# Performance work log

Measured on AMD Instinct MI355X. Metric: run time of the kernel, lower is better.

Reference implementation:

```python
import jax, jax.numpy as jnp
import numpy as np

N, D, E, H = 1024, 256, 16, 8
HD = D // H
F = 4 * D  # GatedMLP intermediate
SCALE = 1.0 / np.sqrt(HD)
EPS = 1e-6


def rmsnorm(x, w):
    rms = jnp.sqrt(jnp.mean(x * x, axis=-1, keepdims=True) + EPS)
    return x / rms * w


def mha(x, wq, wk, wv, wo, mask=None, edge_bias=None):
    # x: [N, D]; weights stored (in, out) so y = x @ W
    q = (x @ wq).reshape(N, H, HD).transpose(1, 0, 2)  # [H, N, HD]
    k = (x @ wk).reshape(N, H, HD).transpose(1, 0, 2)
    v = (x @ wv).reshape(N, H, HD).transpose(1, 0, 2)
    scores = jnp.einsum('hnd,hmd->hnm', q, k) * SCALE  # [H, N, N]
    if edge_bias is not None:
        scores = scores + edge_bias.transpose(2, 0, 1)
    if mask is not None:
        scores = jnp.where(mask[None, :, :], scores, -jnp.inf)
    attn = jax.nn.softmax(scores, axis=-1)
    attn = jnp.nan_to_num(attn, nan=0.0)
    out = jnp.einsum('hnm,hmd->hnd', attn, v)  # [H, N, HD]
    out = out.transpose(1, 0, 2).reshape(N, D)
    return out @ wo


def setup_inputs() -> dict:
    key = jax.random.key(0)
    ks = jax.random.split(key, 40)
    i = iter(range(40))

    def g(shape, s=0.02):
        return (jax.random.normal(ks[next(i)], shape) * s).astype(jnp.float32)

    inp = {
        'features': jax.random.normal(ks[next(i)], (N, D), dtype=jnp.float32),
        'adjacency': jax.random.randint(ks[next(i)], (N, N), 0, 2, dtype=jnp.int32),
        'edge_features': jax.random.normal(ks[next(i)], (N, N, E), dtype=jnp.float32),
        'role_indices': jax.random.randint(ks[next(i)], (N,), 0, 16, dtype=jnp.int64),
        'role_norm_w': jnp.ones((D,), jnp.float32),
        'role_q_w': g((D, D)), 'role_k_w': g((D, D)), 'role_v_w': g((D, D)), 'role_o_w': g((D, D)),
        'nb_norm_w': jnp.ones((D,), jnp.float32),
        'nb_q_w': g((D, D)), 'nb_k_w': g((D, D)), 'nb_v_w': g((D, D)), 'nb_o_w': g((D, D)),
        'edge_w1': g((E, D)), 'edge_b1': jnp.zeros((D,), jnp.float32),
        'edge_w2': g((D, H)), 'edge_b2': jnp.zeros((H,), jnp.float32),
        'full_norm_w': jnp.ones((D,), jnp.float32),
        'full_q_w': g((D, D)), 'full_k_w': g((D, D)), 'full_v_w': g((D, D)), 'full_o_w': g((D, D)),
        'feat_norm_w': jnp.ones((D,), jnp.float32),
        'feat_t_w': g((D, D)), 'feat_t_b': jnp.zeros((D,), jnp.float32),
        'feat_g_w': g((2 * D, D)), 'feat_g_b': jnp.zeros((D,), jnp.float32),
        'ffn_norm_w': jnp.ones((D,), jnp.float32),
        'ffn_gate_w': g((D, F)), 'ffn_up_w': g((D, F)), 'ffn_down_w': g((F, D)),
    }
    return inp


def reference(features, adjacency, edge_features, role_indices,
              role_norm_w, role_q_w, role_k_w, role_v_w, role_o_w,
              nb_norm_w, nb_q_w, nb_k_w, nb_v_w, nb_o_w,
              edge_w1, edge_b1, edge_w2, edge_b2,
              full_norm_w, full_q_w, full_k_w, full_v_w, full_o_w,
              feat_norm_w, feat_t_w, feat_t_b, feat_g_w, feat_g_b,
              ffn_norm_w, ffn_gate_w, ffn_up_w, ffn_down_w):
    # masks (dropout is identity in eval mode)
    role_mask = role_indices[:, None] == role_indices[None, :]          # [N, N]
    neighbor_mask = (adjacency > 0) | jnp.eye(N, dtype=bool)            # [N, N]

    x = features
    # 1. role attention
    x = x + mha(rmsnorm(x, role_norm_w), role_q_w, role_k_w, role_v_w, role_o_w, mask=role_mask)
    # 2. neighbor attention with per-head edge bias from MLP over edge features
    hdn = jax.nn.silu(edge_features @ edge_w1 + edge_b1)                # [N, N, D]
    edge_bias = hdn @ edge_w2 + edge_b2                                 # [N, N, H]
    x = x + mha(rmsnorm(x, nb_norm_w), nb_q_w, nb_k_w, nb_v_w, nb_o_w, mask=neighbor_mask, edge_bias=edge_bias)
    # 3. full attention
    x = x + mha(rmsnorm(x, full_norm_w), full_q_w, full_k_w, full_v_w, full_o_w)
    # 4. feature mixing (gated residual)
    xn = rmsnorm(x, feat_norm_w)
    t = jax.nn.silu(xn @ feat_t_w + feat_t_b)
    gate = jax.nn.sigmoid(jnp.concatenate([xn, t], axis=-1) @ feat_g_w + feat_g_b)
    x = x + gate * t
    # 5. gated FFN
    xn = rmsnorm(x, ffn_norm_w)
    x = x + (jax.nn.silu(xn @ ffn_gate_w) * (xn @ ffn_up_w)) @ ffn_down_w
    return x
```

## Files before the change

### kernel.cpp

```cpp
#include <hip/hip_runtime.h>
#include <math.h>

#define N 1024
#define D 256
#define E 16
#define H 8
#define HD 32
#define F 1024
#define NN (1024 * 1024)
#define SCALE 0.17677669529663687f
#define EPS 1e-6f

typedef unsigned short u16;
typedef __attribute__((ext_vector_type(8))) short bfrag8;
typedef __attribute__((ext_vector_type(4))) float accf4;

__device__ __forceinline__ float block_sum(float v) {
    #pragma unroll
    for (int off = 32; off > 0; off >>= 1) v += __shfl_xor(v, off);
    __shared__ float ws[4];
    if ((threadIdx.x & 63) == 0) ws[threadIdx.x >> 6] = v;
    __syncthreads();
    v = ws[0] + ws[1] + ws[2] + ws[3];
    __syncthreads();
    return v;
}

__device__ __forceinline__ float silu_f(float x) { return x / (1.f + __expf(-x)); }
__device__ __forceinline__ float sigmoid_f(float x) { return 1.f / (1.f + __expf(-x)); }

__device__ __forceinline__ u16 f2bf(float x) {
    union { float f; unsigned int u; } c;
    c.f = x;
    unsigned int r = c.u + 0x7fffu + ((c.u >> 16) & 1u);
    return (u16)(r >> 16);
}

__device__ __forceinline__ unsigned int cvt_pk_bf16(float a, float b) {
    unsigned int r;
    asm("v_cvt_pk_bf16_f32 %0, %1, %2" : "=v"(r) : "v"(a), "v"(b));
    return r;
}

__global__ void copy4_kernel(const float4* __restrict__ a, float4* __restrict__ b, int n4) {
    int i = blockIdx.x * 256 + threadIdx.x;
    if (i < n4) b[i] = a[i];
}

__global__ void gate_combine_kernel(const float* __restrict__ g, const float* __restrict__ t,
                                    float* __restrict__ x, int n) {
    int i = blockIdx.x * 256 + threadIdx.x;
    if (i < n) x[i] += sigmoid_f(g[i]) * t[i];
}

__global__ void cvt_bf16_kernel(const float* __restrict__ in, u16* __restrict__ out, int n) {
    int i = blockIdx.x * 256 + threadIdx.x;
    if (i < n) out[i] = f2bf(in[i]);
}

__global__ void ffn_mulcvt_kernel(const float* __restrict__ guv, u16* __restrict__ hb) {
    int i = blockIdx.x * 256 + threadIdx.x;
    int j = i >> 10, f = i & 1023;
    float g = guv[(long)j * 2048 + f];
    float u = guv[(long)j * 2048 + 1024 + f];
    hb[i] = f2bf(silu_f(g) * u);
}

__global__ void rmsnorm_bf16_kernel(const float* __restrict__ x, const float* __restrict__ w,
                                    u16* __restrict__ out) {
    int row = blockIdx.x;
    int t = threadIdx.x;
    float v = x[(long)row * D + t];
    float s = block_sum(v * v);
    float rms = sqrtf(s * (1.f / D) + EPS);
    out[(long)row * D + t] = f2bf(v / rms * w[t]);
}

__global__ void transpose_bf16_kernel(const float* __restrict__ in, long ldin,
                                      u16* __restrict__ out, int K, int Nc) {
    __shared__ float tile[32][33];
    int k0 = blockIdx.y * 32, n0 = blockIdx.x * 32;
    int c = threadIdx.x & 31, r8 = threadIdx.x >> 5;
    #pragma unroll
    for (int i = 0; i < 4; i++) {
        int r = r8 + i * 8;
        tile[r][c] = in[(long)(k0 + r) * ldin + n0 + c];
    }
    __syncthreads();
    #pragma unroll
    for (int i = 0; i < 4; i++) {
        int r = r8 + i * 8;
        out[(long)(n0 + r) * K + k0 + c] = f2bf(tile[c][r]);
    }
}

template <int NTW, int ACT, bool ACCUM, bool BIAS, bool BF16O>
__global__ __launch_bounds__(256) void bgemm_kernel(
    const u16* __restrict__ A, const u16* __restrict__ B, const float* __restrict__ bias,
    void* __restrict__ C, int M, int K, int Nc, int ldc, long sA, long sB, long sC) {
    constexpr int NTILE = NTW * 16;
    __shared__ __align__(16) u16 Asm[64 * 72];
    __shared__ __align__(16) u16 Bsm[NTILE * 72];
    A += (long)blockIdx.z * sA;
    B += (long)blockIdx.z * sB;
    long cbase = (long)blockIdx.z * sC;
    int m0 = blockIdx.y * 64, n0 = blockIdx.x * NTILE;
    int t = threadIdx.x;
    int wave = t >> 6, lane = t & 63, lg = lane >> 4, lr = lane & 15;
    accf4 acc[NTW] = {};
    for (int k0 = 0; k0 < K; k0 += 64) {
        #pragma unroll
        for (int c = 0; c < 2; c++) {
            int flat = c * 4096 + t * 16;
            int row = flat >> 7, col = (flat & 127) >> 1;
            *(int4*)&Asm[row * 72 + col] = *(const int4*)&A[(long)(m0 + row) * K + k0 + col];
        }
        #pragma unroll
        for (int c = 0; c < NTW / 2; c++) {
            int flat = c * 4096 + t * 16;
            int row = flat >> 7, col = (flat & 127) >> 1;
            *(int4*)&Bsm[row * 72 + col] = *(const int4*)&B[(long)(n0 + row) * K + k0 + col];
        }
        __syncthreads();
        #pragma unroll
        for (int ks = 0; ks < 2; ks++) {
            bfrag8 af = *(const bfrag8*)&Asm[(wave * 16 + lr) * 72 + ks * 32 + lg * 8];
            #pragma unroll
            for (int nt = 0; nt < NTW; nt++) {
                bfrag8 bf = *(const bfrag8*)&Bsm[(nt * 16 + lr) * 72 + ks * 32 + lg * 8];
                acc[nt] = __builtin_amdgcn_mfma_f32_16x16x32_bf16(af, bf, acc[nt], 0, 0, 0);
            }
        }
        __syncthreads();
    }
    float* Cf = (float*)C;
    u16* Cb = (u16*)C;
    #pragma unroll
    for (int nt = 0; nt < NTW; nt++) {
        int gn = n0 + nt * 16 + lr;
        #pragma unroll
        for (int r = 0; r < 4; r++) {
            int gm = m0 + wave * 16 + lg * 4 + r;
            float v = acc[nt][r];
            if (BIAS) v += bias[gn];
            if (ACT == 1) v = silu_f(v);
            long idx = cbase + (long)gm * ldc + gn;
            if (BF16O) Cb[idx] = f2bf(v);
            else if (ACCUM) Cf[idx] += v;
            else Cf[idx] = v;
        }
    }
}

template <int MASK>
__global__ __launch_bounds__(256) void flash_attn_kernel(
    const u16* __restrict__ qkvbf, const u16* __restrict__ vbt,
    const float* __restrict__ ebT, const int* __restrict__ roles,
    const int* __restrict__ adj, u16* __restrict__ aob) {
    __shared__ int roles_s[N];
    __shared__ __align__(16) u16 P_lds[4][16][72];
    __shared__ float mrg_m[4][16], mrg_l[4][16];
    __shared__ __align__(16) float mrg_O[2][32][16];

    int h = blockIdx.y;
    int t = threadIdx.x, wave = t >> 6, lane = t & 63;
    int lg = lane >> 4, lr = lane & 15;
    int iw = wave >> 1, jh = wave & 1;
    int i = blockIdx.x * 32 + iw * 16 + lr;

    if (MASK == 1) {
        #pragma unroll
        for (int c = 0; c < 4; c++) roles_s[t + c * 256] = roles[t + c * 256];
    }
    __syncthreads();

    bfrag8 qf = *(const bfrag8*)&qkvbf[(long)i * 768 + h * HD + lg * 8];
    int role_i = (MASK == 1) ? roles_s[i] : 0;

    accf4 o0 = {0.f, 0.f, 0.f, 0.f}, o1 = {0.f, 0.f, 0.f, 0.f};
    float m_run = -1e30f, l_run = 0.f;

    for (int jt = 0; jt < 8; jt++) {
        int j0 = jh * 512 + jt * 64;
        float p[16];
        float tmax = -1e30f;
        #pragma unroll
        for (int js = 0; js < 4; js++) {
            bfrag8 kf = *(const bfrag8*)&qkvbf[(long)(j0 + js * 16 + lr) * 768 + 256 + h * HD + lg * 8];
            accf4 z = {0.f, 0.f, 0.f, 0.f};
            accf4 s = __builtin_amdgcn_mfma_f32_16x16x32_bf16(kf, qf, z, 0, 0, 0);
            float4 eb4;
            int4 ad4;
            if (MASK == 2) {
                eb4 = *(const float4*)&ebT[(long)h * NN + (long)i * N + j0 + js * 16 + lg * 4];
                ad4 = *(const int4*)&adj[(long)i * N + j0 + js * 16 + lg * 4];
            }
            #pragma unroll
            for (int r = 0; r < 4; r++) {
                int j = j0 + js * 16 + lg * 4 + r;
                float val = s[r] * SCALE;
                bool keep = true;
                if (MASK == 2) {
                    val += (r == 0) ? eb4.x : (r == 1) ? eb4.y : (r == 2) ? eb4.z : eb4.w;
                    int av = (r == 0) ? ad4.x : (r == 1) ? ad4.y : (r == 2) ? ad4.z : ad4.w;
                    keep = (av > 0) || (i == j);
                }
                if (MASK == 1) keep = (roles_s[j] == role_i);
                val = keep ? val : -1e30f;
                p[js * 4 + r] = val;
                tmax = fmaxf(tmax, val);
            }
        }
        tmax = fmaxf(tmax, __shfl_xor(tmax, 16));
        tmax = fmaxf(tmax, __shfl_xor(tmax, 32));
        float m_new = fmaxf(m_run, tmax);
        float alpha = __expf(m_run - m_new);
        float lsum = 0.f;
        #pragma unroll
        for (int v = 0; v < 16; v++) {
            float pe = __expf(p[v] - m_new);
            p[v] = pe;
            lsum += pe;
        }
        lsum += __shfl_xor(lsum, 16);
        lsum += __shfl_xor(lsum, 32);
        l_run = l_run * alpha + lsum;
        m_run = m_new;
        #pragma unroll
        for (int r = 0; r < 4; r++) { o0[r] *= alpha; o1[r] *= alpha; }
        #pragma unroll
        for (int js = 0; js < 4; js++) {
            uint2 pk;
            pk.x = cvt_pk_bf16(p[js * 4 + 0], p[js * 4 + 1]);
            pk.y = cvt_pk_bf16(p[js * 4 + 2], p[js * 4 + 3]);
            *(uint2*)&P_lds[wave][lr][js * 16 + lg * 4] = pk;
        }
        #pragma unroll
        for (int ks = 0; ks < 2; ks++) {
            bfrag8 pb = *(const bfrag8*)&P_lds[wave][lr][ks * 32 + lg * 8];
            bfrag8 v0 = *(const bfrag8*)&vbt[(long)(h * HD + lr) * N + j0 + ks * 32 + lg * 8];
            bfrag8 v1 = *(const bfrag8*)&vbt[(long)(h * HD + 16 + lr) * N + j0 + ks * 32 + lg * 8];
            o0 = __builtin_amdgcn_mfma_f32_16x16x32_bf16(v0, pb, o0, 0, 0, 0);
            o1 = __builtin_amdgcn_mfma_f32_16x16x32_bf16(v1, pb, o1, 0, 0, 0);
        }
    }

    if (lg == 0) { mrg_m[wave][lr] = m_run; mrg_l[wave][lr] = l_run; }
    __syncthreads();
    int other = wave ^ 1;
    float m_o = mrg_m[other][lr], l_o = mrg_l[other][lr];
    float m_tot = fmaxf(m_run, m_o);
    float a_s = __expf(m_run - m_tot);
    float a_o = __expf(m_o - m_tot);
    float inv = 1.f / (a_s * l_run + a_o * l_o);
    if (jh == 0) {
        #pragma unroll
        for (int r = 0; r < 4; r++) {
            mrg_O[iw][lg * 4 + r][lr] = a_s * o0[r];
            mrg_O[iw][16 + lg * 4 + r][lr] = a_s * o1[r];
        }
    }
    __syncthreads();
    if (jh == 1) {
        #pragma unroll
        for (int r = 0; r < 4; r++) {
            float f0 = (mrg_O[iw][lg * 4 + r][lr] + a_s * o0[r]) * inv;
            float f1 = (mrg_O[iw][16 + lg * 4 + r][lr] + a_s * o1[r]) * inv;
            aob[(long)i * D + h * HD + lg * 4 + r] = f2bf(f0);
            aob[(long)i * D + h * HD + 16 + lg * 4 + r] = f2bf(f1);
        }
    }
}

__global__ __launch_bounds__(256, 3) void edge_mlp_mfma_kernel(
    const float* __restrict__ ef, const float* __restrict__ w1, const float* __restrict__ b1,
    const float* __restrict__ w2, const float* __restrict__ b2, float* __restrict__ ebT) {
    __shared__ __align__(16) u16 w1t[256 * 16];
    __shared__ __align__(16) u16 w2t[16 * 256];
    __shared__ __align__(16) u16 hid[4][16 * 264];
    int t = threadIdx.x;
    int i = blockIdx.x;

    {
        int d = t;
        #pragma unroll
        for (int e = 0; e < 16; e++) w1t[d * 16 + e] = f2bf(w1[e * 256 + d]);
        float4 wa = *(const float4*)&w2[d * 8];
        float4 wb = *(const float4*)&w2[d * 8 + 4];
        w2t[0 * 256 + d] = f2bf(wa.x);
        w2t[1 * 256 + d] = f2bf(wa.y);
        w2t[2 * 256 + d] = f2bf(wa.z);
        w2t[3 * 256 + d] = f2bf(wa.w);
        w2t[4 * 256 + d] = f2bf(wb.x);
        w2t[5 * 256 + d] = f2bf(wb.y);
        w2t[6 * 256 + d] = f2bf(wb.z);
        w2t[7 * 256 + d] = f2bf(wb.w);
        #pragma unroll
        for (int h = 8; h < 16; h++) w2t[h * 256 + d] = 0;
    }
    __syncthreads();

    int wave = t >> 6, lane = t & 63;
    int lg = lane >> 4, lr = lane & 15;
    u16* hw = hid[wave];

    bfrag8 a1[16];
    #pragma unroll
    for (int dt = 0; dt < 16; dt++) {
        int d = dt * 16 + lr;
        if (lg < 2) {
            a1[dt] = *(const bfrag8*)&w1t[d * 16 + lg * 8];
        } else if (lg == 2) {
            union { unsigned int u[4]; bfrag8 s; } z = {{0u, 0u, 0u, 0u}};
            z.u[0] = (unsigned int)f2bf(b1[d]);
            a1[dt] = z.s;
        } else {
            union { unsigned int u[4]; bfrag8 s; } z = {{0u, 0u, 0u, 0u}};
            a1[dt] = z.s;
        }
    }
    bfrag8 a2[8];
    #pragma unroll
    for (int ks = 0; ks < 8; ks++)
        a2[ks] = *(const bfrag8*)&w2t[lr * 256 + ks * 32 + lg * 8];

    float b2v[4];
    #pragma unroll
    for (int r = 0; r < 4; r++) b2v[r] = (lg < 2) ? b2[lg * 4 + r] : 0.f;

    for (int it = 0; it < 16; it++) {
        long rowbase = (long)i * N + (it * 4 + wave) * 16;
        bfrag8 bfrag;
        if (lg < 2) {
            const float* p = &ef[(rowbase + lr) * E + lg * 8];
            float4 f0 = *(const float4*)p;
            float4 f1 = *(const float4*)(p + 4);
            union { unsigned int u[4]; bfrag8 s; } uu;
            uu.u[0] = cvt_pk_bf16(f0.x, f0.y);
            uu.u[1] = cvt_pk_bf16(f0.z, f0.w);
            uu.u[2] = cvt_pk_bf16(f1.x, f1.y);
            uu.u[3] = cvt_pk_bf16(f1.z, f1.w);
            bfrag = uu.s;
        } else {
            union { unsigned int u[4]; bfrag8 s; } uu = {{(lg == 2) ? 0x3f80u : 0u, 0u, 0u, 0u}};
            bfrag = uu.s;
        }
        #pragma unroll
        for (int dt = 0; dt < 16; dt++) {
            accf4 acc = {0.f, 0.f, 0.f, 0.f};
            acc = __builtin_amdgcn_mfma_f32_16x16x32_bf16(a1[dt], bfrag, acc, 0, 0, 0);
            float s0 = silu_f(acc[0]);
            float s1 = silu_f(acc[1]);
            float s2 = silu_f(acc[2]);
            float s3 = silu_f(acc[3]);
            uint2 pk;
            pk.x = cvt_pk_bf16(s0, s1);
            pk.y = cvt_pk_bf16(s2, s3);
            *(uint2*)&hw[lr * 264 + dt * 16 + lg * 4] = pk;
        }
        accf4 acc2 = {0.f, 0.f, 0.f, 0.f};
        #pragma unroll
        for (int ks = 0; ks < 8; ks++) {
            bfrag8 hb = *(const bfrag8*)&hw[lr * 264 + ks * 32 + lg * 8];
            acc2 = __builtin_amdgcn_mfma_f32_16x16x32_bf16(a2[ks], hb, acc2, 0, 0, 0);
        }
        if (lg < 2) {
            #pragma unroll
            for (int r = 0; r < 4; r++)
                ebT[(long)(lg * 4 + r) * NN + rowbase + lr] = acc2[r] + b2v[r];
        }
    }
}

extern "C" void kernel_launch(void* const* d_in, const int* in_sizes, int n_in,
                              void* d_out, int out_size, void* d_ws, size_t ws_size,
                              hipStream_t stream) {
    const float* features   = (const float*)d_in[0];
    const int*   adjacency  = (const int*)d_in[1];
    const float* edge_feats = (const float*)d_in[2];
    const int*   role_idx   = (const int*)d_in[3];
    const float* role_norm_w = (const float*)d_in[4];
    const float* role_q_w = (const float*)d_in[5];
    const float* role_k_w = (const float*)d_in[6];
    const float* role_v_w = (const float*)d_in[7];
    const float* role_o_w = (const float*)d_in[8];
    const float* nb_norm_w = (const float*)d_in[9];
    const float* nb_q_w = (const float*)d_in[10];
    const float* nb_k_w = (const float*)d_in[11];
    const float* nb_v_w = (const float*)d_in[12];
    const float* nb_o_w = (const float*)d_in[13];
    const float* edge_w1 = (const float*)d_in[14];
    const float* edge_b1 = (const float*)d_in[15];
    const float* edge_w2 = (const float*)d_in[16];
    const float* edge_b2 = (const float*)d_in[17];
    const float* full_norm_w = (const float*)d_in[18];
    const float* full_q_w = (const float*)d_in[19];
    const float* full_k_w = (const float*)d_in[20];
    const float* full_v_w = (const float*)d_in[21];
    const float* full_o_w = (const float*)d_in[22];
    const float* feat_norm_w = (const float*)d_in[23];
    const float* feat_t_w = (const float*)d_in[24];
    const float* feat_t_b = (const float*)d_in[25];
    const float* feat_g_w = (const float*)d_in[26];
    const float* feat_g_b = (const float*)d_in[27];
    const float* ffn_norm_w = (const float*)d_in[28];
    const float* ffn_gate_w = (const float*)d_in[29];
    const float* ffn_up_w = (const float*)d_in[30];
    const float* ffn_down_w = (const float*)d_in[31];

    char* wsp = (char*)d_ws;
    size_t off = 0;
    auto alloc = [&](size_t bytes) -> void* {
        void* p = wsp + off;
        off += (bytes + 255) & ~(size_t)255;
        return p;
    };
    float* x    = (float*)alloc((size_t)N * D * 4);
    float* qkvb = (float*)alloc((size_t)N * 768 * 4);
    float* ao   = (float*)alloc((size_t)N * D * 4);
    float* tmp  = (float*)alloc((size_t)N * D * 4);
    float* eb   = (float*)alloc((size_t)H * NN * 4);
    float* guv  = (float*)alloc((size_t)N * 2048 * 4);
    u16* qkvbf = (u16*)alloc((size_t)N * 768 * 2);
    u16* aob  = (u16*)alloc((size_t)N * D * 2);
    u16* xnb  = (u16*)alloc((size_t)N * D * 2);
    u16* tb   = (u16*)alloc((size_t)N * D * 2);
    u16* hb   = (u16*)alloc((size_t)N * F * 2);
    u16* vbt  = (u16*)alloc((size_t)D * N * 2);
    u16* wqkvt[3];
    u16* wot[3];
    for (int a = 0; a < 3; a++) {
        wqkvt[a] = (u16*)alloc((size_t)768 * 256 * 2);
        wot[a]   = (u16*)alloc((size_t)256 * 256 * 2);
    }
    u16* wtt  = (u16*)alloc((size_t)256 * 256 * 2);
    u16* wg1t = (u16*)alloc((size_t)256 * 256 * 2);
    u16* wg2t = (u16*)alloc((size_t)256 * 256 * 2);
    u16* wgut = (u16*)alloc((size_t)2048 * 256 * 2);
    u16* wdt  = (u16*)alloc((size_t)256 * 1024 * 2);

    auto tr = [&](const float* in, long ldin, u16* out, int K, int Nc) {
        transpose_bf16_kernel<<<dim3(Nc / 32, K / 32), 256, 0, stream>>>(in, ldin, out, K, Nc);
    };

    const float* qw[3] = {role_q_w, nb_q_w, full_q_w};
    const float* kw[3] = {role_k_w, nb_k_w, full_k_w};
    const float* vw[3] = {role_v_w, nb_v_w, full_v_w};
    const float* ow[3] = {role_o_w, nb_o_w, full_o_w};
    for (int a = 0; a < 3; a++) {
        tr(qw[a], D, wqkvt[a], D, D);
        tr(kw[a], D, wqkvt[a] + 256 * 256, D, D);
        tr(vw[a], D, wqkvt[a] + 512 * 256, D, D);
        tr(ow[a], D, wot[a], D, D);
    }
    tr(feat_t_w, D, wtt, D, D);
    tr(feat_g_w, D, wg1t, D, D);
    tr(feat_g_w + (size_t)D * D, D, wg2t, D, D);
    tr(ffn_gate_w, F, wgut, D, F);
    tr(ffn_up_w, F, wgut + (size_t)F * 256, D, F);
    tr(ffn_down_w, D, wdt, F, D);

    copy4_kernel<<<(N * D / 4) / 256, 256, 0, stream>>>((const float4*)features, (float4*)x, N * D / 4);
    edge_mlp_mfma_kernel<<<N, 256, 0, stream>>>(edge_feats, edge_w1, edge_b1, edge_w2, edge_b2, eb);

    const float* nw[3] = {role_norm_w, nb_norm_w, full_norm_w};
    dim3 fgrid(N / 32, H);

    for (int a = 0; a < 3; a++) {
        rmsnorm_bf16_kernel<<<N, 256, 0, stream>>>(x, nw[a], xnb);
        bgemm_kernel<4, 0, false, false, false><<<dim3(768 / 64, N / 64, 1), 256, 0, stream>>>(
            xnb, wqkvt[a], nullptr, qkvb, N, 256, 768, 768, 0, 0, 0);
        cvt_bf16_kernel<<<(N * 768) / 256, 256, 0, stream>>>(qkvb, qkvbf, N * 768);
        tr(qkvb + 512, 768, vbt, N, D);
        if (a == 0)
            flash_attn_kernel<1><<<fgrid, 256, 0, stream>>>(qkvbf, vbt, nullptr, role_idx, nullptr, aob);
        else if (a == 1)
            flash_attn_kernel<2><<<fgrid, 256, 0, stream>>>(qkvbf, vbt, eb, nullptr, adjacency, aob);
        else
            flash_attn_kernel<0><<<fgrid, 256, 0, stream>>>(qkvbf, vbt, nullptr, nullptr, nullptr, aob);
        bgemm_kernel<4, 0, true, false, false><<<dim3(D / 64, N / 64, 1), 256, 0, stream>>>(
            aob, wot[a], nullptr, x, N, 256, D, D, 0, 0, 0);
    }

    rmsnorm_bf16_kernel<<<N, 256, 0, stream>>>(x, feat_norm_w, xnb);
    bgemm_kernel<4, 1, false, true, false><<<dim3(D / 64, N / 64, 1), 256, 0, stream>>>(
        xnb, wtt, feat_t_b, ao, N, 256, D, D, 0, 0, 0);
    cvt_bf16_kernel<<<(N * D) / 256, 256, 0, stream>>>(ao, tb, N * D);
    bgemm_kernel<4, 0, false, true, false><<<dim3(D / 64, N / 64, 1), 256, 0, stream>>>(
        xnb, wg1t, feat_g_b, tmp, N, 256, D, D, 0, 0, 0);
    bgemm_kernel<4, 0, true, false, false><<<dim3(D / 64, N / 64, 1), 256, 0, stream>>>(
        tb, wg2t, nullptr, tmp, N, 256, D, D, 0, 0, 0);
    gate_combine_kernel<<<(N * D) / 256, 256, 0, stream>>>(tmp, ao, x, N * D);

    rmsnorm_bf16_kernel<<<N, 256, 0, stream>>>(x, ffn_norm_w, xnb);
    bgemm_kernel<4, 0, false, false, false><<<dim3(2048 / 64, N / 64, 1), 256, 0, stream>>>(
        xnb, wgut, nullptr, guv, N, 256, 2048, 2048, 0, 0, 0);
    ffn_mulcvt_kernel<<<(N * F) / 256, 256, 0, stream>>>(guv, hb);
    bgemm_kernel<4, 0, true, false, false><<<dim3(D / 64, N / 64, 1), 256, 0, stream>>>(
        hb, wdt, nullptr, x, N, 1024, D, D, 0, 0, 0);
    copy4_kernel<<<(N * D / 4) / 256, 256, 0, stream>>>((const float4*)x, (float4*)d_out, N * D / 4);
}
```

Before: 537.9 us.

## Emit bf16 GEMM outputs directly, batch weight transposes, prefetch edge features

The QKV, feature-transform and FFN gate/up GEMMs now write bf16 directly, which removes the separate fp32→bf16 conversion kernels and halves their intermediate traffic. The V transpose now reads bf16. The many per-weight transpose launches are merged into three batched launches. The edge-MLP kernel reuses one shared buffer for weights and hidden tiles, drops its occupancy hint, prefetches the next edge-feature tile into registers, and hoists the hidden-fragment LDS reads ahead of the MFMAs. The cost is extra rounding: the gate/up values and t are now rounded to bf16 before the elementwise ops.

New measurement: 491.4 us. 1.09x faster.

```diff
diff --git a/kernel.cpp b/kernel.cpp
--- a/kernel.cpp
+++ b/kernel.cpp
@@ -36,6 +36,12 @@
     return (u16)(r >> 16);
 }
 
+__device__ __forceinline__ float bf2f(u16 v) {
+    union { unsigned int u; float f; } c;
+    c.u = ((unsigned int)v) << 16;
+    return c.f;
+}
+
 __device__ __forceinline__ unsigned int cvt_pk_bf16(float a, float b) {
     unsigned int r;
     asm("v_cvt_pk_bf16_f32 %0, %1, %2" : "=v"(r) : "v"(a), "v"(b));
@@ -47,22 +53,17 @@
     if (i < n4) b[i] = a[i];
 }
 
-__global__ void gate_combine_kernel(const float* __restrict__ g, const float* __restrict__ t,
+__global__ void gate_combine_kernel(const float* __restrict__ g, const u16* __restrict__ t,
                                     float* __restrict__ x, int n) {
     int i = blockIdx.x * 256 + threadIdx.x;
-    if (i < n) x[i] += sigmoid_f(g[i]) * t[i];
-}
-
-__global__ void cvt_bf16_kernel(const float* __restrict__ in, u16* __restrict__ out, int n) {
-    int i = blockIdx.x * 256 + threadIdx.x;
-    if (i < n) out[i] = f2bf(in[i]);
-}
-
-__global__ void ffn_mulcvt_kernel(const float* __restrict__ guv, u16* __restrict__ hb) {
+    if (i < n) x[i] += sigmoid_f(g[i]) * bf2f(t[i]);
+}
+
+__global__ void ffn_mulcvt_kernel(const u16* __restrict__ guv, u16* __restrict__ hb) {
     int i = blockIdx.x * 256 + threadIdx.x;
     int j = i >> 10, f = i & 1023;
-    float g = guv[(long)j * 2048 + f];
-    float u = guv[(long)j * 2048 + 1024 + f];
+    float g = bf2f(guv[(long)j * 2048 + f]);
+    float u = bf2f(guv[(long)j * 2048 + 1024 + f]);
     hb[i] = f2bf(silu_f(g) * u);
 }
 
@@ -91,6 +92,64 @@
     for (int i = 0; i < 4; i++) {
         int r = r8 + i * 8;
         out[(long)(n0 + r) * K + k0 + c] = f2bf(tile[c][r]);
+    }
+}
+
+struct Src15 { const float* p[15]; };
+__global__ void transpose15_kernel(Src15 srcs, u16* __restrict__ wall) {
+    __shared__ float tile[32][33];
+    const float* in = srcs.p[blockIdx.z];
+    u16* out = wall + (size_t)blockIdx.z * 65536;
+    int k0 = blockIdx.y * 32, n0 = blockIdx.x * 32;
+    int c = threadIdx.x & 31, r8 = threadIdx.x >> 5;
+    #pragma unroll
+    for (int i = 0; i < 4; i++) {
+        int r = r8 + i * 8;
+        tile[r][c] = in[(long)(k0 + r) * 256 + n0 + c];
+    }
+    __syncthreads();
+    #pragma unroll
+    for (int i = 0; i < 4; i++) {
+        int r = r8 + i * 8;
+        out[(long)(n0 + r) * 256 + k0 + c] = f2bf(tile[c][r]);
+    }
+}
+
+struct Src2 { const float* p[2]; };
+__global__ void transpose_gu_kernel(Src2 srcs, u16* __restrict__ wgut) {
+    __shared__ float tile[32][33];
+    const float* in = srcs.p[blockIdx.z];
+    u16* out = wgut + (size_t)blockIdx.z * (size_t)F * 256;
+    int k0 = blockIdx.y * 32, n0 = blockIdx.x * 32;
+    int c = threadIdx.x & 31, r8 = threadIdx.x >> 5;
+    #pragma unroll
+    for (int i = 0; i < 4; i++) {
+        int r = r8 + i * 8;
+        tile[r][c] = in[(long)(k0 + r) * F + n0 + c];
+    }
+    __syncthreads();
+    #pragma unroll
+    for (int i = 0; i < 4; i++) {
+        int r = r8 + i * 8;
+        out[(long)(n0 + r) * 256 + k0 + c] = f2bf(tile[c][r]);
+    }
+}
+
+__global__ void transpose_u16_kernel(const u16* __restrict__ in, long ldin,
+                                     u16* __restrict__ out, int K, int Nc) {
+    __shared__ u16 tile[32][34];
+    int k0 = blockIdx.y * 32, n0 = blockIdx.x * 32;
+    int c = threadIdx.x & 31, r8 = threadIdx.x >> 5;
+    #pragma unroll
+    for (int i = 0; i < 4; i++) {
+        int r = r8 + i * 8;
+        tile[r][c] = in[(long)(k0 + r) * ldin + n0 + c];
+    }
+    __syncthreads();
+    #pragma unroll
+    for (int i = 0; i < 4; i++) {
+        int r = r8 + i * 8;
+        out[(long)(n0 + r) * K + k0 + c] = tile[c][r];
     }
 }
 
@@ -272,12 +331,12 @@
     }
 }
 
-__global__ __launch_bounds__(256, 3) void edge_mlp_mfma_kernel(
+__global__ __launch_bounds__(256) void edge_mlp_mfma_kernel(
     const float* __restrict__ ef, const float* __restrict__ w1, const float* __restrict__ b1,
     const float* __restrict__ w2, const float* __restrict__ b2, float* __restrict__ ebT) {
-    __shared__ __align__(16) u16 w1t[256 * 16];
-    __shared__ __align__(16) u16 w2t[16 * 256];
-    __shared__ __align__(16) u16 hid[4][16 * 264];
+    __shared__ __align__(16) u16 smem[4][16 * 264];
+    u16* w1t = &smem[0][0];
+    u16* w2t = w1t + 4096;
     int t = threadIdx.x;
     int i = blockIdx.x;
 
@@ -302,7 +361,6 @@
 
     int wave = t >> 6, lane = t & 63;
     int lg = lane >> 4, lr = lane & 15;
-    u16* hw = hid[wave];
 
     bfrag8 a1[16];
     #pragma unroll
@@ -328,13 +386,20 @@
     #pragma unroll
     for (int r = 0; r < 4; r++) b2v[r] = (lg < 2) ? b2[lg * 4 + r] : 0.f;
 
+    __syncthreads();
+    u16* hw = smem[wave];
+
+    float4 f0, f1;
+    if (lg < 2) {
+        const float* p = &ef[((long)i * N + wave * 16 + lr) * E + lg * 8];
+        f0 = *(const float4*)p;
+        f1 = *(const float4*)(p + 4);
+    }
+
     for (int it = 0; it < 16; it++) {
         long rowbase = (long)i * N + (it * 4 + wave) * 16;
         bfrag8 bfrag;
         if (lg < 2) {
-            const float* p = &ef[(rowbase + lr) * E + lg * 8];
-            float4 f0 = *(const float4*)p;
-            float4 f1 = *(const float4*)(p + 4);
             union { unsigned int u[4]; bfrag8 s; } uu;
             uu.u[0] = cvt_pk_bf16(f0.x, f0.y);
             uu.u[1] = cvt_pk_bf16(f0.z, f0.w);
@@ -344,6 +409,11 @@
         } else {
             union { unsigned int u[4]; bfrag8 s; } uu = {{(lg == 2) ? 0x3f80u : 0u, 0u, 0u, 0u}};
             bfrag = uu.s;
+        }
+        if (it < 15 && lg < 2) {
+            const float* p = &ef[((long)i * N + ((it + 1) * 4 + wave) * 16 + lr) * E + lg * 8];
+            f0 = *(const float4*)p;
+            f1 = *(const float4*)(p + 4);
         }
         #pragma unroll
         for (int dt = 0; dt < 16; dt++) {
@@ -358,12 +428,14 @@
             pk.y = cvt_pk_bf16(s2, s3);
             *(uint2*)&hw[lr * 264 + dt * 16 + lg * 4] = pk;
         }
+        bfrag8 hbv[8];
+        #pragma unroll
+        for (int ks = 0; ks < 8; ks++)
+            hbv[ks] = *(const bfrag8*)&hw[lr * 264 + ks * 32 + lg * 8];
         accf4 acc2 = {0.f, 0.f, 0.f, 0.f};
         #pragma unroll
-        for (int ks = 0; ks < 8; ks++) {
-            bfrag8 hb = *(const bfrag8*)&hw[lr * 264 + ks * 32 + lg * 8];
-            acc2 = __builtin_amdgcn_mfma_f32_16x16x32_bf16(a2[ks], hb, acc2, 0, 0, 0);
-        }
+        for (int ks = 0; ks < 8; ks++)
+            acc2 = __builtin_amdgcn_mfma_f32_16x16x32_bf16(a2[ks], hbv[ks], acc2, 0, 0, 0);
         if (lg < 2) {
             #pragma unroll
             for (int r = 0; r < 4; r++)
@@ -416,49 +488,38 @@
         return p;
     };
     float* x    = (float*)alloc((size_t)N * D * 4);
-    float* qkvb = (float*)alloc((size_t)N * 768 * 4);
-    float* ao   = (float*)alloc((size_t)N * D * 4);
     float* tmp  = (float*)alloc((size_t)N * D * 4);
     float* eb   = (float*)alloc((size_t)H * NN * 4);
-    float* guv  = (float*)alloc((size_t)N * 2048 * 4);
     u16* qkvbf = (u16*)alloc((size_t)N * 768 * 2);
+    u16* guvb = (u16*)alloc((size_t)N * 2048 * 2);
     u16* aob  = (u16*)alloc((size_t)N * D * 2);
     u16* xnb  = (u16*)alloc((size_t)N * D * 2);
     u16* tb   = (u16*)alloc((size_t)N * D * 2);
     u16* hb   = (u16*)alloc((size_t)N * F * 2);
     u16* vbt  = (u16*)alloc((size_t)D * N * 2);
-    u16* wqkvt[3];
-    u16* wot[3];
-    for (int a = 0; a < 3; a++) {
-        wqkvt[a] = (u16*)alloc((size_t)768 * 256 * 2);
-        wot[a]   = (u16*)alloc((size_t)256 * 256 * 2);
-    }
-    u16* wtt  = (u16*)alloc((size_t)256 * 256 * 2);
-    u16* wg1t = (u16*)alloc((size_t)256 * 256 * 2);
-    u16* wg2t = (u16*)alloc((size_t)256 * 256 * 2);
+    u16* wall = (u16*)alloc((size_t)15 * 65536 * 2);
     u16* wgut = (u16*)alloc((size_t)2048 * 256 * 2);
     u16* wdt  = (u16*)alloc((size_t)256 * 1024 * 2);
 
-    auto tr = [&](const float* in, long ldin, u16* out, int K, int Nc) {
-        transpose_bf16_kernel<<<dim3(Nc / 32, K / 32), 256, 0, stream>>>(in, ldin, out, K, Nc);
-    };
-
-    const float* qw[3] = {role_q_w, nb_q_w, full_q_w};
-    const float* kw[3] = {role_k_w, nb_k_w, full_k_w};
-    const float* vw[3] = {role_v_w, nb_v_w, full_v_w};
-    const float* ow[3] = {role_o_w, nb_o_w, full_o_w};
+    u16* wqkvt[3], *wot[3];
     for (int a = 0; a < 3; a++) {
-        tr(qw[a], D, wqkvt[a], D, D);
-        tr(kw[a], D, wqkvt[a] + 256 * 256, D, D);
-        tr(vw[a], D, wqkvt[a] + 512 * 256, D, D);
-        tr(ow[a], D, wot[a], D, D);
-    }
-    tr(feat_t_w, D, wtt, D, D);
-    tr(feat_g_w, D, wg1t, D, D);
-    tr(feat_g_w + (size_t)D * D, D, wg2t, D, D);
-    tr(ffn_gate_w, F, wgut, D, F);
-    tr(ffn_up_w, F, wgut + (size_t)F * 256, D, F);
-    tr(ffn_down_w, D, wdt, F, D);
+        wqkvt[a] = wall + (size_t)(a * 4) * 65536;
+        wot[a]   = wall + (size_t)(a * 4 + 3) * 65536;
+    }
+    u16* wtt  = wall + (size_t)12 * 65536;
+    u16* wg1t = wall + (size_t)13 * 65536;
+    u16* wg2t = wall + (size_t)14 * 65536;
+
+    Src15 s15;
+    s15.p[0] = role_q_w;  s15.p[1] = role_k_w;  s15.p[2] = role_v_w;  s15.p[3] = role_o_w;
+    s15.p[4] = nb_q_w;    s15.p[5] = nb_k_w;    s15.p[6] = nb_v_w;    s15.p[7] = nb_o_w;
+    s15.p[8] = full_q_w;  s15.p[9] = full_k_w;  s15.p[10] = full_v_w; s15.p[11] = full_o_w;
+    s15.p[12] = feat_t_w; s15.p[13] = feat_g_w; s15.p[14] = feat_g_w + (size_t)D * D;
+    transpose15_kernel<<<dim3(8, 8, 15), 256, 0, stream>>>(s15, wall);
+    Src2 s2;
+    s2.p[0] = ffn_gate_w; s2.p[1] = ffn_up_w;
+    transpose_gu_kernel<<<dim3(32, 8, 2), 256, 0, stream>>>(s2, wgut);
+    transpose_bf16_kernel<<<dim3(8, 32), 256, 0, stream>>>(ffn_down_w, D, wdt, F, D);
 
     copy4_kernel<<<(N * D / 4) / 256, 256, 0, stream>>>((const float4*)features, (float4*)x, N * D / 4);
     edge_mlp_mfma_kernel<<<N, 256, 0, stream>>>(edge_feats, edge_w1, edge_b1, edge_w2, edge_b2, eb);
@@ -468,10 +529,9 @@
 
     for (int a = 0; a < 3; a++) {
         rmsnorm_bf16_kernel<<<N, 256, 0, stream>>>(x, nw[a], xnb);
-        bgemm_kernel<4, 0, false, false, false><<<dim3(768 / 64, N / 64, 1), 256, 0, stream>>>(
-            xnb, wqkvt[a], nullptr, qkvb, N, 256, 768, 768, 0, 0, 0);
-        cvt_bf16_kernel<<<(N * 768) / 256, 256, 0, stream>>>(qkvb, qkvbf, N * 768);
-        tr(qkvb + 512, 768, vbt, N, D);
+        bgemm_kernel<4, 0, false, false, true><<<dim3(768 / 64, N / 64, 1), 256, 0, stream>>>(
+            xnb, wqkvt[a], nullptr, qkvbf, N, 256, 768, 768, 0, 0, 0);
+        transpose_u16_kernel<<<dim3(8, 32), 256, 0, stream>>>(qkvbf + 512, 768, vbt, N, D);
         if (a == 0)
             flash_attn_kernel<1><<<fgrid, 256, 0, stream>>>(qkvbf, vbt, nullptr, role_idx, nullptr, aob);
         else if (a == 1)
@@ -483,19 +543,18 @@
     }
 
     rmsnorm_bf16_kernel<<<N, 256, 0, stream>>>(x, feat_norm_w, xnb);
-    bgemm_kernel<4, 1, false, true, false><<<dim3(D / 64, N / 64, 1), 256, 0, stream>>>(
-        xnb, wtt, feat_t_b, ao, N, 256, D, D, 0, 0, 0);
-    cvt_bf16_kernel<<<(N * D) / 256, 256, 0, stream>>>(ao, tb, N * D);
+    bgemm_kernel<4, 1, false, true, true><<<dim3(D / 64, N / 64, 1), 256, 0, stream>>>(
+        xnb, wtt, feat_t_b, tb, N, 256, D, D, 0, 0, 0);
     bgemm_kernel<4, 0, false, true, false><<<dim3(D / 64, N / 64, 1), 256, 0, stream>>>(
         xnb, wg1t, feat_g_b, tmp, N, 256, D, D, 0, 0, 0);
     bgemm_kernel<4, 0, true, false, false><<<dim3(D / 64, N / 64, 1), 256, 0, stream>>>(
         tb, wg2t, nullptr, tmp, N, 256, D, D, 0, 0, 0);
-    gate_combine_kernel<<<(N * D) / 256, 256, 0, stream>>>(tmp, ao, x, N * D);
+    gate_combine_kernel<<<(N * D) / 256, 256, 0, stream>>>(tmp, tb, x, N * D);
 
     rmsnorm_bf16_kernel<<<N, 256, 0, stream>>>(x, ffn_norm_w, xnb);
-    bgemm_kernel<4, 0, false, false, false><<<dim3(2048 / 64, N / 64, 1), 256, 0, stream>>>(
-        xnb, wgut, nullptr, guv, N, 256, 2048, 2048, 0, 0, 0);
-    ffn_mulcvt_kernel<<<(N * F) / 256, 256, 0, stream>>>(guv, hb);
+    bgemm_kernel<4, 0, false, false, true><<<dim3(2048 / 64, N / 64, 1), 256, 0, stream>>>(
+        xnb, wgut, nullptr, guvb, N, 256, 2048, 2048, 0, 0, 0);
+    ffn_mulcvt_kernel<<<(N * F) / 256, 256, 0, stream>>>(guvb, hb);
     bgemm_kernel<4, 0, true, false, false><<<dim3(D / 64, N / 64, 1), 256, 0, stream>>>(
         hb, wdt, nullptr, x, N, 1024, D, D, 0, 0, 0);
     copy4_kernel<<<(N * D / 4) / 256, 256, 0, stream>>>((const float4*)x, (float4*)d_out, N * D / 4);
```
